# Kernel optimization log

Hardware: AMD Instinct MI355X
Metric: run time of the kernel (lower is better)

## Reference

```python
import jax, jax.numpy as jnp
import numpy as np

B, D, N, K, H = 8, 1024, 4096, 64, 512


def setup_inputs() -> dict:
    key = jax.random.key(0)
    ks = jax.random.split(key, 8)
    s1 = 1.0 / np.sqrt(D)
    s2 = 1.0 / np.sqrt(H)
    return {
        "feature": jax.random.normal(ks[0], (B, D, N), jnp.float32),
        "xyz": jax.random.normal(ks[1], (B, 3, N), jnp.float32),
        "w1": jax.random.normal(ks[2], (H, D), jnp.float32) * s1,
        "b1": jnp.zeros((H,), jnp.float32),
        "g1": jnp.ones((H,), jnp.float32),
        "be1": jnp.zeros((H,), jnp.float32),
        "w2": jax.random.normal(ks[3], (H, H), jnp.float32) * s2,
        "b2": jnp.zeros((H,), jnp.float32),
        "g2": jnp.ones((H,), jnp.float32),
        "be2": jnp.zeros((H,), jnp.float32),
        "w3": jax.random.normal(ks[4], (K, H), jnp.float32) * s2,
        "b3": jnp.zeros((K,), jnp.float32),
    }


def _conv1d(x, w, b):
    # pointwise Conv1d (kernel_size=1): [b,c,n] x [o,c] -> [b,o,n]
    return jnp.einsum('bcn,oc->bon', x, w) + b[None, :, None]


def _bn(x, g, be, eps=1e-5):
    # BatchNorm1d in training mode: batch statistics over (batch, spatial)
    m = x.mean(axis=(0, 2), keepdims=True)
    v = x.var(axis=(0, 2), keepdims=True)
    return (x - m) * jax.lax.rsqrt(v + eps) * g[None, :, None] + be[None, :, None]


def _regular(center, reg=1e-4):
    k = center.shape[-1]
    gram = jnp.einsum('bdm,bdn->bmn', center, center)
    return reg * jnp.abs(gram - jnp.eye(k, dtype=center.dtype)[None]).mean()


def _sinkhorn(cost, epsilon, max_iter):
    # log-domain Sinkhorn with uniform marginals; fixed iteration count
    b, n, m = cost.shape
    log_p = jnp.full((b, n), -np.log(n), cost.dtype)
    log_q = jnp.full((b, m), -np.log(m), cost.dtype)

    def M(u, v):
        return (-cost + u[:, :, None] + v[:, None, :]) / epsilon

    def body(i, uv):
        u, v = uv
        u = epsilon * (log_p - jax.nn.logsumexp(M(u, v), axis=-1)) + u
        v = epsilon * (log_q - jax.nn.logsumexp(M(u, v), axis=-2)) + v
        return (u, v)

    u0 = jnp.zeros((b, n), cost.dtype)
    v0 = jnp.zeros((b, m), cost.dtype)
    u, v = jax.lax.fori_loop(0, max_iter, body, (u0, v0))
    return jnp.exp(M(u, v))  # transport plan gamma [b,n,m]


def _ot_assign(x, y, epsilon=1e-3, max_iter=25, dst='fe'):
    # x: [b,d,n], y: [b,d,m]
    if dst == 'eu':
        xn = jnp.sum(x * x, axis=1)  # [b,n]
        yn = jnp.sum(y * y, axis=1)  # [b,m]
        cost = xn[:, :, None] + yn[:, None, :] - 2.0 * jnp.einsum('bdn,bdm->bnm', x, y)
    else:
        cost = 2.0 - 2.0 * jnp.einsum('bdn,bdm->bnm', x, y)
    return _sinkhorn(cost, epsilon, max_iter)


def _normalize(x, axis=1, eps=1e-12):
    nrm = jnp.linalg.norm(x, axis=axis, keepdims=True)
    return x / jnp.maximum(nrm, eps)


def reference(feature, xyz, w1, b1, g1, be1, w2, b2, g2, be2, w3, b3):
    b, d, n = feature.shape
    h = jax.nn.relu(_bn(_conv1d(feature, w1, b1), g1, be1))
    h = jax.nn.relu(_bn(_conv1d(h, w2, b2), g2, be2))
    log_score = _conv1d(h, w3, b3)  # [b,K,n]
    score = jax.nn.softmax(log_score, axis=1)
    pi = jax.lax.stop_gradient(jnp.maximum(score.sum(-1), 1e-4))[:, None, :]  # [b,1,K]

    # xyz branch
    mu_xyz = jnp.einsum('bkn,bdn->bdk', score, xyz) / pi  # [b,3,K]
    reg_xyz = 0.001 * _regular(mu_xyz)
    gamma_xyz = _ot_assign(jax.lax.stop_gradient(xyz), jax.lax.stop_gradient(mu_xyz), dst='eu')
    assign_xyz = jax.lax.stop_gradient(n * jnp.swapaxes(gamma_xyz, -1, -2))  # [b,K,n]

    # feature branch
    mu_fea = jnp.einsum('bkn,bdn->bdk', score, feature) / pi  # [b,D,K]
    n_feature = _normalize(feature)
    n_mu = _normalize(mu_fea)
    reg_fea = _regular(n_mu)
    gamma_fea = _ot_assign(jax.lax.stop_gradient(n_feature), jax.lax.stop_gradient(n_mu), dst='fe')
    assign_fea = jax.lax.stop_gradient(n * jnp.swapaxes(gamma_fea, -1, -2))  # [b,K,n]

    logp = jax.nn.log_softmax(log_score, axis=1)
    loss_xyz = -jnp.mean(jnp.sum(assign_xyz * logp, axis=1))
    loss_fea = -jnp.mean(jnp.sum(assign_fea * logp, axis=1))
    return loss_xyz + loss_fea + reg_fea + reg_xyz
```

## Files before the change

kernel.cpp:

```cpp
#include <hip/hip_runtime.h>
#include <math.h>

#define B_ 8
#define D_ 1024
#define N_ 4096
#define K_ 64
#define H_ 512

typedef short sx8 __attribute__((ext_vector_type(8)));
typedef float fx4 __attribute__((ext_vector_type(4)));

__device__ __forceinline__ float block_reduce_sum256(float v, float* sm) {
  int tid = threadIdx.x;
  sm[tid] = v;
  __syncthreads();
  for (int s = 128; s > 0; s >>= 1) {
    if (tid < s) sm[tid] += sm[tid + s];
    __syncthreads();
  }
  float r = sm[0];
  __syncthreads();
  return r;
}

__device__ __forceinline__ float bf2f(ushort h) {
  return __uint_as_float(((unsigned)h) << 16);
}
__device__ __forceinline__ void split2(float f, ushort& h, ushort& l) {
  unsigned u = __float_as_uint(f);
  float hf = __uint_as_float(u & 0xffff0000u);
  h = (ushort)(u >> 16);
  l = (ushort)(__float_as_uint(f - hf) >> 16);
}

__global__ __launch_bounds__(256)
void split_w3(const float* __restrict__ W1, const float* __restrict__ W2,
              const float* __restrict__ W3, ushort* __restrict__ Wh1,
              ushort* __restrict__ Wl1, ushort* __restrict__ Wh2,
              ushort* __restrict__ Wl2, ushort* __restrict__ Wh3,
              ushort* __restrict__ Wl3) {
  int i = blockIdx.x * 256 + threadIdx.x;
  const float* W;
  ushort *Wh, *Wl;
  int o;
  if (i < 524288) { W = W1; Wh = Wh1; Wl = Wl1; o = i; }
  else if (i < 786432) { W = W2; Wh = Wh2; Wl = Wl2; o = i - 524288; }
  else { W = W3; Wh = Wh3; Wl = Wl3; o = i - 786432; }
  ushort h, l;
  split2(W[o], h, l);
  Wh[o] = h;
  Wl[o] = l;
}

__global__ __launch_bounds__(256)
void conv_bt128(const ushort* __restrict__ Ah, const ushort* __restrict__ Al,
                const float* __restrict__ Bf, const float* __restrict__ scale,
                const float* __restrict__ shift, float* __restrict__ C,
                const float* __restrict__ bias, float* __restrict__ rs,
                float* __restrict__ rss, float* __restrict__ nrm,
                int Kd, long sB, long sC) {
  __shared__ ushort As[2][128][40];
  __shared__ ushort Bs[2][128][40];
  __shared__ float Ft[32][132];
  __shared__ float scb[32], shb[32];
  __shared__ float rs_l[128], rss_l[128];
  const int t = threadIdx.x;
  const int n0 = blockIdx.x * 128;
  const int m0 = blockIdx.y * 128;
  const int b = blockIdx.z;
  const float* Fsrc = Bf + (long)b * sB;
  float* Cp = C + (long)b * sC;
  const int half = t >> 7, rA = t & 127;
  const ushort* Asrc = (half ? Al : Ah) + (long)(m0 + rA) * Kd;
  ushort* AsD = &As[half][rA][0];
  const int dr = t >> 3, cc = (t & 7) * 16;
  const int nl = t & 127, dh = t >> 7;
  const int w = t >> 6, ln = t & 15, qd = (t & 63) >> 4;
  const int wm = w >> 1, wn = w & 1;
  if (t < 128) { rs_l[t] = 0.f; rss_l[t] = 0.f; }
  float nsq = 0.f;

  fx4 acc[4][4];
#pragma unroll
  for (int i = 0; i < 4; ++i)
#pragma unroll
    for (int j = 0; j < 4; ++j) acc[i][j] = (fx4)0.f;

  for (int k0 = 0; k0 < Kd; k0 += 32) {
    float4 f0 = *(const float4*)(Fsrc + (long)(k0 + dr) * N_ + n0 + cc);
    float4 f1 = *(const float4*)(Fsrc + (long)(k0 + dr) * N_ + n0 + cc + 4);
    float4 f2 = *(const float4*)(Fsrc + (long)(k0 + dr) * N_ + n0 + cc + 8);
    float4 f3 = *(const float4*)(Fsrc + (long)(k0 + dr) * N_ + n0 + cc + 12);
    uint4 a0 = *(const uint4*)(Asrc + k0);
    uint4 a1 = *(const uint4*)(Asrc + k0 + 8);
    uint4 a2 = *(const uint4*)(Asrc + k0 + 16);
    uint4 a3 = *(const uint4*)(Asrc + k0 + 24);
    __syncthreads();
    *(float4*)&Ft[dr][cc] = f0;
    *(float4*)&Ft[dr][cc + 4] = f1;
    *(float4*)&Ft[dr][cc + 8] = f2;
    *(float4*)&Ft[dr][cc + 12] = f3;
    *(uint4*)(AsD + 0) = a0;
    *(uint4*)(AsD + 8) = a1;
    *(uint4*)(AsD + 16) = a2;
    *(uint4*)(AsD + 24) = a3;
    if (t < 32) {
      scb[t] = scale ? scale[k0 + t] : 1.f;
      shb[t] = scale ? shift[k0 + t] : 0.f;
    }
    __syncthreads();
    sx8 hv0, hv1, lv0, lv1;
#pragma unroll
    for (int j = 0; j < 8; ++j) {
      float v = Ft[dh * 16 + j][nl];
      if (scale) v = fmaxf(v * scb[dh * 16 + j] + shb[dh * 16 + j], 0.f);
      nsq += v * v;
      ushort h, l;
      split2(v, h, l);
      hv0[j] = (short)h;
      lv0[j] = (short)l;
    }
#pragma unroll
    for (int j = 0; j < 8; ++j) {
      float v = Ft[dh * 16 + 8 + j][nl];
      if (scale) v = fmaxf(v * scb[dh * 16 + 8 + j] + shb[dh * 16 + 8 + j], 0.f);
      nsq += v * v;
      ushort h, l;
      split2(v, h, l);
      hv1[j] = (short)h;
      lv1[j] = (short)l;
    }
    *(sx8*)&Bs[0][nl][dh * 16] = hv0;
    *(sx8*)&Bs[0][nl][dh * 16 + 8] = hv1;
    *(sx8*)&Bs[1][nl][dh * 16] = lv0;
    *(sx8*)&Bs[1][nl][dh * 16 + 8] = lv1;
    __syncthreads();
    sx8 ahf[4], alf[4], bhf[4], blf[4];
#pragma unroll
    for (int mt = 0; mt < 4; ++mt) {
      ahf[mt] = *(const sx8*)&As[0][wm * 64 + mt * 16 + ln][qd * 8];
      alf[mt] = *(const sx8*)&As[1][wm * 64 + mt * 16 + ln][qd * 8];
    }
#pragma unroll
    for (int nt = 0; nt < 4; ++nt) {
      bhf[nt] = *(const sx8*)&Bs[0][wn * 64 + nt * 16 + ln][qd * 8];
      blf[nt] = *(const sx8*)&Bs[1][wn * 64 + nt * 16 + ln][qd * 8];
    }
#pragma unroll
    for (int mt = 0; mt < 4; ++mt)
#pragma unroll
      for (int nt = 0; nt < 4; ++nt) {
        acc[mt][nt] = __builtin_amdgcn_mfma_f32_16x16x32_bf16(ahf[mt], bhf[nt], acc[mt][nt], 0, 0, 0);
        acc[mt][nt] = __builtin_amdgcn_mfma_f32_16x16x32_bf16(alf[mt], bhf[nt], acc[mt][nt], 0, 0, 0);
        acc[mt][nt] = __builtin_amdgcn_mfma_f32_16x16x32_bf16(ahf[mt], blf[nt], acc[mt][nt], 0, 0, 0);
      }
  }
#pragma unroll
  for (int mt = 0; mt < 4; ++mt) {
#pragma unroll
    for (int rr = 0; rr < 4; ++rr) {
      int rloc = wm * 64 + mt * 16 + qd * 4 + rr;
      int row = m0 + rloc;
      float bb = bias[row];
      float s1 = 0.f, s2 = 0.f;
#pragma unroll
      for (int nt = 0; nt < 4; ++nt) {
        int col = n0 + wn * 64 + nt * 16 + ln;
        float y = acc[mt][nt][rr] + bb;
        Cp[(long)row * N_ + col] = y;
        s1 += y;
        s2 += y * y;
      }
      if (rs) {
#pragma unroll
        for (int m = 1; m < 16; m <<= 1) {
          s1 += __shfl_xor(s1, m);
          s2 += __shfl_xor(s2, m);
        }
        if (ln == 0) {
          atomicAdd(&rs_l[rloc], s1);
          atomicAdd(&rss_l[rloc], s2);
        }
      }
    }
  }
  if (nrm && blockIdx.y == 0)
    atomicAdd(&nrm[(long)b * N_ + n0 + nl], nsq);
  if (rs) {
    __syncthreads();
    if (t < 128) {
      atomicAdd(&rs[m0 + t], rs_l[t]);
      atomicAdd(&rss[m0 + t], rss_l[t]);
    }
  }
}

__global__ void bn_fin(const float* __restrict__ rs, const float* __restrict__ rss,
                       const float* __restrict__ g, const float* __restrict__ be,
                       float* __restrict__ sc, float* __restrict__ sh) {
  int c = blockIdx.x * 256 + threadIdx.x;
  if (c < H_) {
    float inv = 1.f / (float)(B_ * N_);
    float m = rs[c] * inv;
    float var = rss[c] * inv - m * m;
    float s = g[c] * rsqrtf(var + 1e-5f);
    sc[c] = s;
    sh[c] = be[c] - m * s;
  }
}

__global__ __launch_bounds__(256)
void conv64_bn(const ushort* __restrict__ Ah, const ushort* __restrict__ Al,
               const float* __restrict__ Bf, const float* __restrict__ scale,
               const float* __restrict__ shift, float* __restrict__ C,
               const float* __restrict__ bias, int Kd, long sB, long sC) {
  __shared__ ushort As[2][64][40];
  __shared__ ushort Bs[2][128][40];
  __shared__ float Ft[32][132];
  __shared__ float scb[32], shb[32];
  const int t = threadIdx.x;
  const int n0 = blockIdx.x * 128;
  const int b = blockIdx.z;
  const float* Fsrc = Bf + (long)b * sB;
  float* Cp = C + (long)b * sC;
  const bool doA = t < 128;
  const int hA = (t >> 6) & 1, rA = t & 63;
  const ushort* Asrc = (hA ? Al : Ah) + (long)rA * Kd;
  ushort* AsD = &As[hA][rA][0];
  const int dr = t >> 3, cc = (t & 7) * 16;
  const int nl = t & 127, dh = t >> 7;
  const int w = t >> 6, ln = t & 15, qd = (t & 63) >> 4;
  const int wm = w >> 1, wn = w & 1;

  fx4 acc[2][4];
#pragma unroll
  for (int i = 0; i < 2; ++i)
#pragma unroll
    for (int j = 0; j < 4; ++j) acc[i][j] = (fx4)0.f;

  for (int k0 = 0; k0 < Kd; k0 += 32) {
    float4 f0 = *(const float4*)(Fsrc + (long)(k0 + dr) * N_ + n0 + cc);
    float4 f1 = *(const float4*)(Fsrc + (long)(k0 + dr) * N_ + n0 + cc + 4);
    float4 f2 = *(const float4*)(Fsrc + (long)(k0 + dr) * N_ + n0 + cc + 8);
    float4 f3 = *(const float4*)(Fsrc + (long)(k0 + dr) * N_ + n0 + cc + 12);
    uint4 a0, a1, a2, a3;
    if (doA) {
      a0 = *(const uint4*)(Asrc + k0);
      a1 = *(const uint4*)(Asrc + k0 + 8);
      a2 = *(const uint4*)(Asrc + k0 + 16);
      a3 = *(const uint4*)(Asrc + k0 + 24);
    }
    __syncthreads();
    *(float4*)&Ft[dr][cc] = f0;
    *(float4*)&Ft[dr][cc + 4] = f1;
    *(float4*)&Ft[dr][cc + 8] = f2;
    *(float4*)&Ft[dr][cc + 12] = f3;
    if (doA) {
      *(uint4*)(AsD + 0) = a0;
      *(uint4*)(AsD + 8) = a1;
      *(uint4*)(AsD + 16) = a2;
      *(uint4*)(AsD + 24) = a3;
    }
    if (t < 32) {
      scb[t] = scale[k0 + t];
      shb[t] = shift[k0 + t];
    }
    __syncthreads();
    sx8 hv0, hv1, lv0, lv1;
#pragma unroll
    for (int j = 0; j < 8; ++j) {
      float v = Ft[dh * 16 + j][nl];
      v = fmaxf(v * scb[dh * 16 + j] + shb[dh * 16 + j], 0.f);
      ushort h, l;
      split2(v, h, l);
      hv0[j] = (short)h;
      lv0[j] = (short)l;
    }
#pragma unroll
    for (int j = 0; j < 8; ++j) {
      float v = Ft[dh * 16 + 8 + j][nl];
      v = fmaxf(v * scb[dh * 16 + 8 + j] + shb[dh * 16 + 8 + j], 0.f);
      ushort h, l;
      split2(v, h, l);
      hv1[j] = (short)h;
      lv1[j] = (short)l;
    }
    *(sx8*)&Bs[0][nl][dh * 16] = hv0;
    *(sx8*)&Bs[0][nl][dh * 16 + 8] = hv1;
    *(sx8*)&Bs[1][nl][dh * 16] = lv0;
    *(sx8*)&Bs[1][nl][dh * 16 + 8] = lv1;
    __syncthreads();
    sx8 ahf[2], alf[2], bhf[4], blf[4];
#pragma unroll
    for (int mt = 0; mt < 2; ++mt) {
      ahf[mt] = *(const sx8*)&As[0][wm * 32 + mt * 16 + ln][qd * 8];
      alf[mt] = *(const sx8*)&As[1][wm * 32 + mt * 16 + ln][qd * 8];
    }
#pragma unroll
    for (int nt = 0; nt < 4; ++nt) {
      bhf[nt] = *(const sx8*)&Bs[0][wn * 64 + nt * 16 + ln][qd * 8];
      blf[nt] = *(const sx8*)&Bs[1][wn * 64 + nt * 16 + ln][qd * 8];
    }
#pragma unroll
    for (int mt = 0; mt < 2; ++mt)
#pragma unroll
      for (int nt = 0; nt < 4; ++nt) {
        acc[mt][nt] = __builtin_amdgcn_mfma_f32_16x16x32_bf16(ahf[mt], bhf[nt], acc[mt][nt], 0, 0, 0);
        acc[mt][nt] = __builtin_amdgcn_mfma_f32_16x16x32_bf16(alf[mt], bhf[nt], acc[mt][nt], 0, 0, 0);
        acc[mt][nt] = __builtin_amdgcn_mfma_f32_16x16x32_bf16(ahf[mt], blf[nt], acc[mt][nt], 0, 0, 0);
      }
  }
#pragma unroll
  for (int mt = 0; mt < 2; ++mt)
#pragma unroll
    for (int rr = 0; rr < 4; ++rr) {
      int row = wm * 32 + mt * 16 + qd * 4 + rr;
      float bb = bias[row];
#pragma unroll
      for (int nt = 0; nt < 4; ++nt) {
        int col = n0 + wn * 64 + nt * 16 + ln;
        Cp[(long)row * N_ + col] = acc[mt][nt][rr] + bb;
      }
    }
}

__global__ __launch_bounds__(256)
void gemm64_bf(const ushort* __restrict__ Ah, const ushort* __restrict__ Al,
               const float* __restrict__ Bf, float* __restrict__ Cacc) {
  __shared__ ushort As[2][64][40];
  __shared__ ushort Bs[2][128][40];
  const int t = threadIdx.x;
  const int nc0 = blockIdx.x * 128;
  const int kBeg = blockIdx.y * 1024;
  const int b = blockIdx.z;
  const int pc = t >> 7, rB = t & 127;
  const float* Bsrc = Bf + (long)b * D_ * N_ + (long)(nc0 + rB) * N_ + kBeg + pc * 16;
  const bool doA = t < 128;
  const int hA = (t >> 6) & 1, rA = t & 63;
  const ushort* Asrc = (hA ? Al : Ah) + (long)b * K_ * N_ + (long)rA * N_ + kBeg;
  ushort* AsD = &As[hA][rA][0];
  const int w = t >> 6, ln = t & 15, qd = (t & 63) >> 4;
  const int wm = w >> 1, wn = w & 1;

  fx4 acc[2][4];
#pragma unroll
  for (int i = 0; i < 2; ++i)
#pragma unroll
    for (int j = 0; j < 4; ++j) acc[i][j] = (fx4)0.f;

  for (int k0 = 0; k0 < 1024; k0 += 32) {
    float4 f0 = *(const float4*)(Bsrc + k0);
    float4 f1 = *(const float4*)(Bsrc + k0 + 4);
    float4 f2 = *(const float4*)(Bsrc + k0 + 8);
    float4 f3 = *(const float4*)(Bsrc + k0 + 12);
    uint4 a0, a1, a2, a3;
    if (doA) {
      a0 = *(const uint4*)(Asrc + k0);
      a1 = *(const uint4*)(Asrc + k0 + 8);
      a2 = *(const uint4*)(Asrc + k0 + 16);
      a3 = *(const uint4*)(Asrc + k0 + 24);
    }
    float fv[16] = {f0.x, f0.y, f0.z, f0.w, f1.x, f1.y, f1.z, f1.w,
                    f2.x, f2.y, f2.z, f2.w, f3.x, f3.y, f3.z, f3.w};
    sx8 hv0, hv1, lv0, lv1;
#pragma unroll
    for (int j = 0; j < 8; ++j) {
      ushort h, l;
      split2(fv[j], h, l);
      hv0[j] = (short)h;
      lv0[j] = (short)l;
    }
#pragma unroll
    for (int j = 0; j < 8; ++j) {
      ushort h, l;
      split2(fv[8 + j], h, l);
      hv1[j] = (short)h;
      lv1[j] = (short)l;
    }
    __syncthreads();
    *(sx8*)&Bs[0][rB][pc * 16] = hv0;
    *(sx8*)&Bs[0][rB][pc * 16 + 8] = hv1;
    *(sx8*)&Bs[1][rB][pc * 16] = lv0;
    *(sx8*)&Bs[1][rB][pc * 16 + 8] = lv1;
    if (doA) {
      *(uint4*)(AsD + 0) = a0;
      *(uint4*)(AsD + 8) = a1;
      *(uint4*)(AsD + 16) = a2;
      *(uint4*)(AsD + 24) = a3;
    }
    __syncthreads();
    sx8 ahf[2], alf[2], bhf[4], blf[4];
#pragma unroll
    for (int mt = 0; mt < 2; ++mt) {
      ahf[mt] = *(const sx8*)&As[0][wm * 32 + mt * 16 + ln][qd * 8];
      alf[mt] = *(const sx8*)&As[1][wm * 32 + mt * 16 + ln][qd * 8];
    }
#pragma unroll
    for (int nt = 0; nt < 4; ++nt) {
      bhf[nt] = *(const sx8*)&Bs[0][wn * 64 + nt * 16 + ln][qd * 8];
      blf[nt] = *(const sx8*)&Bs[1][wn * 64 + nt * 16 + ln][qd * 8];
    }
#pragma unroll
    for (int mt = 0; mt < 2; ++mt)
#pragma unroll
      for (int nt = 0; nt < 4; ++nt) {
        acc[mt][nt] = __builtin_amdgcn_mfma_f32_16x16x32_bf16(ahf[mt], bhf[nt], acc[mt][nt], 0, 0, 0);
        acc[mt][nt] = __builtin_amdgcn_mfma_f32_16x16x32_bf16(alf[mt], bhf[nt], acc[mt][nt], 0, 0, 0);
        acc[mt][nt] = __builtin_amdgcn_mfma_f32_16x16x32_bf16(ahf[mt], blf[nt], acc[mt][nt], 0, 0, 0);
      }
  }
#pragma unroll
  for (int mt = 0; mt < 2; ++mt)
#pragma unroll
    for (int rr = 0; rr < 4; ++rr) {
      int row = wm * 32 + mt * 16 + qd * 4 + rr;
#pragma unroll
      for (int nt = 0; nt < 4; ++nt) {
        int col = nc0 + wn * 64 + nt * 16 + ln;
        atomicAdd(&Cacc[((long)b * K_ + row) * D_ + col], acc[mt][nt][rr]);
      }
    }
}

__global__ __launch_bounds__(256)
void gemm64_bt(const ushort* __restrict__ Ah, const ushort* __restrict__ Al,
               const float* __restrict__ Bf, const float* __restrict__ nrmsq,
               float* __restrict__ cost) {
  __shared__ ushort As[2][64][40];
  __shared__ ushort Bs[2][128][40];
  __shared__ float Ft[32][132];
  const int t = threadIdx.x;
  const int n0 = blockIdx.x * 128;
  const int b = blockIdx.z;
  const float* Fsrc = Bf + (long)b * D_ * N_;
  const bool doA = t < 128;
  const int hA = (t >> 6) & 1, rA = t & 63;
  const ushort* Asrc = (hA ? Al : Ah) + (long)b * K_ * D_ + (long)rA * D_;
  ushort* AsD = &As[hA][rA][0];
  const int dr = t >> 3, cc = (t & 7) * 16;
  const int nl = t & 127, dh = t >> 7;
  const int w = t >> 6, ln = t & 15, qd = (t & 63) >> 4;
  const int wm = w >> 1, wn = w & 1;

  fx4 acc[2][4];
#pragma unroll
  for (int i = 0; i < 2; ++i)
#pragma unroll
    for (int j = 0; j < 4; ++j) acc[i][j] = (fx4)0.f;

  for (int k0 = 0; k0 < D_; k0 += 32) {
    float4 f0 = *(const float4*)(Fsrc + (long)(k0 + dr) * N_ + n0 + cc);
    float4 f1 = *(const float4*)(Fsrc + (long)(k0 + dr) * N_ + n0 + cc + 4);
    float4 f2 = *(const float4*)(Fsrc + (long)(k0 + dr) * N_ + n0 + cc + 8);
    float4 f3 = *(const float4*)(Fsrc + (long)(k0 + dr) * N_ + n0 + cc + 12);
    uint4 a0, a1, a2, a3;
    if (doA) {
      a0 = *(const uint4*)(Asrc + k0);
      a1 = *(const uint4*)(Asrc + k0 + 8);
      a2 = *(const uint4*)(Asrc + k0 + 16);
      a3 = *(const uint4*)(Asrc + k0 + 24);
    }
    __syncthreads();
    *(float4*)&Ft[dr][cc] = f0;
    *(float4*)&Ft[dr][cc + 4] = f1;
    *(float4*)&Ft[dr][cc + 8] = f2;
    *(float4*)&Ft[dr][cc + 12] = f3;
    if (doA) {
      *(uint4*)(AsD + 0) = a0;
      *(uint4*)(AsD + 8) = a1;
      *(uint4*)(AsD + 16) = a2;
      *(uint4*)(AsD + 24) = a3;
    }
    __syncthreads();
    sx8 hv0, hv1, lv0, lv1;
#pragma unroll
    for (int j = 0; j < 8; ++j) {
      ushort h, l;
      split2(Ft[dh * 16 + j][nl], h, l);
      hv0[j] = (short)h;
      lv0[j] = (short)l;
    }
#pragma unroll
    for (int j = 0; j < 8; ++j) {
      ushort h, l;
      split2(Ft[dh * 16 + 8 + j][nl], h, l);
      hv1[j] = (short)h;
      lv1[j] = (short)l;
    }
    *(sx8*)&Bs[0][nl][dh * 16] = hv0;
    *(sx8*)&Bs[0][nl][dh * 16 + 8] = hv1;
    *(sx8*)&Bs[1][nl][dh * 16] = lv0;
    *(sx8*)&Bs[1][nl][dh * 16 + 8] = lv1;
    __syncthreads();
    sx8 ahf[2], alf[2], bhf[4], blf[4];
#pragma unroll
    for (int mt = 0; mt < 2; ++mt) {
      ahf[mt] = *(const sx8*)&As[0][wm * 32 + mt * 16 + ln][qd * 8];
      alf[mt] = *(const sx8*)&As[1][wm * 32 + mt * 16 + ln][qd * 8];
    }
#pragma unroll
    for (int nt = 0; nt < 4; ++nt) {
      bhf[nt] = *(const sx8*)&Bs[0][wn * 64 + nt * 16 + ln][qd * 8];
      blf[nt] = *(const sx8*)&Bs[1][wn * 64 + nt * 16 + ln][qd * 8];
    }
#pragma unroll
    for (int mt = 0; mt < 2; ++mt)
#pragma unroll
      for (int nt = 0; nt < 4; ++nt) {
        acc[mt][nt] = __builtin_amdgcn_mfma_f32_16x16x32_bf16(ahf[mt], bhf[nt], acc[mt][nt], 0, 0, 0);
        acc[mt][nt] = __builtin_amdgcn_mfma_f32_16x16x32_bf16(alf[mt], bhf[nt], acc[mt][nt], 0, 0, 0);
        acc[mt][nt] = __builtin_amdgcn_mfma_f32_16x16x32_bf16(ahf[mt], blf[nt], acc[mt][nt], 0, 0, 0);
      }
  }
#pragma unroll
  for (int nt = 0; nt < 4; ++nt) {
    int col = n0 + wn * 64 + nt * 16 + ln;
    float q = nrmsq[b * N_ + col];
    float iv = 1.f / fmaxf(sqrtf(q), 1e-12f);
#pragma unroll
    for (int mt = 0; mt < 2; ++mt)
#pragma unroll
      for (int rr = 0; rr < 4; ++rr) {
        int row = wm * 32 + mt * 16 + qd * 4 + rr;
        cost[((long)b * K_ + row) * N_ + col] = 2.f - 2.f * acc[mt][nt][rr] * iv;
      }
  }
}

__global__ __launch_bounds__(256)
void softmax_nk(const float* __restrict__ ls, ushort* __restrict__ sch,
                ushort* __restrict__ scl, float* __restrict__ logpNK,
                float* __restrict__ pi_raw) {
  __shared__ float L[64][65];
  __shared__ float ploc[64];
  int tid = threadIdx.x;
  if (tid < 64) ploc[tid] = 0.f;
  __syncthreads();
  int bi = blockIdx.x >> 4;
  int nb = (blockIdx.x & 15) * 256;
  int n = nb + tid;
  const float* x = ls + ((long)bi * K_) * N_ + n;
  float xv[64];
#pragma unroll
  for (int k = 0; k < 64; ++k) xv[k] = x[(long)k * N_];
  float mx = -1e30f;
#pragma unroll
  for (int k = 0; k < 64; ++k) mx = fmaxf(mx, xv[k]);
  float s = 0.f;
#pragma unroll
  for (int k = 0; k < 64; ++k) s += __expf(xv[k] - mx);
  float lg = __logf(s);
  float inv = 1.f / s;
#pragma unroll
  for (int k = 0; k < 64; ++k) {
    float sc = __expf(xv[k] - mx) * inv;
    long o = ((long)bi * K_ + k) * N_ + n;
    ushort h, l;
    split2(sc, h, l);
    sch[o] = h;
    scl[o] = l;
    atomicAdd(&ploc[k], sc);
  }
  __syncthreads();
  if (tid < 64) atomicAdd(&pi_raw[bi * 64 + tid], ploc[tid]);
  int myw = tid >> 6, nl = tid & 63;
  int row = tid >> 2, ch = (tid & 3) * 16;
  for (int p = 0; p < 4; ++p) {
    __syncthreads();
    if (myw == p) {
#pragma unroll
      for (int k = 0; k < 64; ++k) L[nl][k] = xv[k] - mx - lg;
    }
    __syncthreads();
    float o0[16];
#pragma unroll
    for (int j = 0; j < 16; ++j) o0[j] = L[row][ch + j];
    float* dst = logpNK + ((long)bi * N_ + nb + p * 64 + row) * 64 + ch;
    *(float4*)(dst + 0) = make_float4(o0[0], o0[1], o0[2], o0[3]);
    *(float4*)(dst + 4) = make_float4(o0[4], o0[5], o0[6], o0[7]);
    *(float4*)(dst + 8) = make_float4(o0[8], o0[9], o0[10], o0[11]);
    *(float4*)(dst + 12) = make_float4(o0[12], o0[13], o0[14], o0[15]);
  }
}

__global__ __launch_bounds__(64)
void mu_xyz_k(const ushort* __restrict__ sch, const ushort* __restrict__ scl,
              const float* __restrict__ xyz, const float* __restrict__ pi_raw,
              float* __restrict__ mu, float* __restrict__ yn) {
  int k = blockIdx.x, b = blockIdx.y, t = threadIdx.x;
  const ushort* sh = sch + ((long)b * K_ + k) * N_;
  const ushort* sl = scl + ((long)b * K_ + k) * N_;
  const float* xp = xyz + (long)b * 3 * N_;
  float a0 = 0, a1 = 0, a2 = 0;
  for (int n = t; n < N_; n += 64) {
    float s = bf2f(sh[n]) + bf2f(sl[n]);
    a0 += s * xp[n];
    a1 += s * xp[N_ + n];
    a2 += s * xp[2 * N_ + n];
  }
  for (int off = 32; off > 0; off >>= 1) {
    a0 += __shfl_down(a0, off);
    a1 += __shfl_down(a1, off);
    a2 += __shfl_down(a2, off);
  }
  if (t == 0) {
    float p = fmaxf(pi_raw[b * K_ + k], 1e-4f);
    float m0 = a0 / p, m1 = a1 / p, m2 = a2 / p;
    mu[((long)b * 3 + 0) * K_ + k] = m0;
    mu[((long)b * 3 + 1) * K_ + k] = m1;
    mu[((long)b * 3 + 2) * K_ + k] = m2;
    yn[b * K_ + k] = m0 * m0 + m1 * m1 + m2 * m2;
  }
}

__global__ __launch_bounds__(256)
void reg_xyz_k(const float* __restrict__ mu, float* __restrict__ out) {
  __shared__ float red[256];
  int b = blockIdx.x, tid = threadIdx.x;
  float acc = 0.f;
  for (int e = tid; e < 4096; e += 256) {
    int m = e >> 6, n2 = e & 63;
    float g = 0.f;
    for (int d = 0; d < 3; ++d)
      g += mu[((long)b * 3 + d) * K_ + m] * mu[((long)b * 3 + d) * K_ + n2];
    acc += fabsf(g - (m == n2 ? 1.f : 0.f));
  }
  float tot = block_reduce_sum256(acc, red);
  if (tid == 0) atomicAdd(out, tot * (1e-7f / 32768.f));
}

__global__ __launch_bounds__(256)
void reg_fea_k(const float* __restrict__ nT, float* __restrict__ out) {
  __shared__ float pm[1024];
  __shared__ float red[256];
  int m = blockIdx.x, b = blockIdx.y, tid = threadIdx.x;
  const float* base = nT + (long)b * K_ * D_;
  *(float4*)&pm[tid * 4] = *(const float4*)(base + (long)m * D_ + tid * 4);
  __syncthreads();
  int n2 = tid >> 2, q = tid & 3;
  const float* pn = base + (long)n2 * D_ + q * 256;
  const float* pml = &pm[q * 256];
  float g = 0.f;
#pragma unroll 8
  for (int d = 0; d < 256; d += 4) {
    float4 v = *(const float4*)(pn + d);
    g += v.x * pml[d] + v.y * pml[d + 1] + v.z * pml[d + 2] + v.w * pml[d + 3];
  }
  g += __shfl_down(g, 2);
  g += __shfl_down(g, 1);
  float acc = (q == 0) ? fabsf(g - (m == n2 ? 1.f : 0.f)) : 0.f;
  float tot = block_reduce_sum256(acc, red);
  if (tid == 0) atomicAdd(out, tot * (1e-4f / 32768.f));
}

__global__ __launch_bounds__(256)
void mu_finalize(const float* __restrict__ muT_raw, const float* __restrict__ pi_raw,
                 float* __restrict__ n_muT, ushort* __restrict__ nmu_h,
                 ushort* __restrict__ nmu_l) {
  __shared__ float red[256];
  int k = blockIdx.x, b = blockIdx.y, tid = threadIdx.x;
  float p = fmaxf(pi_raw[b * K_ + k], 1e-4f);
  const float* src = muT_raw + ((long)b * K_ + k) * D_;
  float ss = 0.f;
  for (int d = tid; d < D_; d += 256) {
    float v = src[d] / p;
    ss += v * v;
  }
  float tot = block_reduce_sum256(ss, red);
  float inv = 1.f / fmaxf(sqrtf(tot), 1e-12f);
  long o = ((long)b * K_ + k) * D_;
  for (int d = tid; d < D_; d += 256) {
    float v = src[d] / p * inv;
    n_muT[o + d] = v;
    ushort h, l;
    split2(v, h, l);
    nmu_h[o + d] = h;
    nmu_l[o + d] = l;
  }
}

__global__ __launch_bounds__(256, 1)
void sinkhorn_coop(const float* __restrict__ cost_f, const float* __restrict__ xyz,
                   const float* __restrict__ mu, const float* __restrict__ yn,
                   const float* __restrict__ logpNK, float* __restrict__ out,
                   unsigned long long* __restrict__ partMS,
                   unsigned int* __restrict__ seq) {
  __shared__ float tile[4][64][68];
  __shared__ float vsh[64];
  __shared__ float wm[4][64];
  __shared__ float wsum[4][64];
  __shared__ float red[256];
  __shared__ float mub[4][64];
  const int tid = threadIdx.x;
  const int g = blockIdx.x & 15;
  const int s = blockIdx.x >> 4;
  const int w = tid >> 6, lane = tid & 63;
  const int i = s * 256 + tid;
  const int b = g & 7;
  const float eps = 1e-3f, ti = 1000.0f;
  const float lgp = -8.317766166719343f;
  const float lgq = -4.1588830833596715f;

  float c[64];
  if (g < 8) {
    if (tid < 64) {
      mub[0][tid] = mu[(b * 3 + 0) * K_ + tid];
      mub[1][tid] = mu[(b * 3 + 1) * K_ + tid];
      mub[2][tid] = mu[(b * 3 + 2) * K_ + tid];
      mub[3][tid] = yn[b * K_ + tid];
      vsh[tid] = 0.f;
    }
    __syncthreads();
    float x0 = xyz[((long)b * 3 + 0) * N_ + i];
    float x1 = xyz[((long)b * 3 + 1) * N_ + i];
    float x2 = xyz[((long)b * 3 + 2) * N_ + i];
    float xn = x0 * x0 + x1 * x1 + x2 * x2;
#pragma unroll
    for (int j = 0; j < 64; ++j)
      c[j] = xn + mub[3][j] - 2.f * (x0 * mub[0][j] + x1 * mub[1][j] + x2 * mub[2][j]);
  } else {
    const float* C = cost_f + (long)b * K_ * N_;
#pragma unroll
    for (int j = 0; j < 64; ++j) c[j] = C[(long)j * N_ + i];
    if (tid < 64) vsh[tid] = 0.f;
    __syncthreads();
  }
  float u = 0.f;

  for (int it = 0; it < 25; ++it) {
    float tj[64];
#pragma unroll
    for (int j = 0; j < 64; ++j) tj[j] = vsh[j] - c[j];
    float dm = -1e30f;
#pragma unroll
    for (int j = 0; j < 64; ++j) dm = fmaxf(dm, tj[j]);
    float ssum = 0.f;
#pragma unroll
    for (int j = 0; j < 64; ++j) ssum += __expf((tj[j] - dm) * ti);
    u = eps * (lgp - ((u + dm) * ti + __logf(ssum))) + u;
#pragma unroll
    for (int j4 = 0; j4 < 16; ++j4) {
      float4 v4;
      v4.x = (u + tj[j4 * 4 + 0]) * ti;
      v4.y = (u + tj[j4 * 4 + 1]) * ti;
      v4.z = (u + tj[j4 * 4 + 2]) * ti;
      v4.w = (u + tj[j4 * 4 + 3]) * ti;
      *(float4*)&tile[w][lane][j4 * 4] = v4;
    }
    __syncthreads();
    float M = -1e30f, S = 0.f;
#pragma unroll
    for (int r = 0; r < 64; ++r) {
      float a = tile[w][r][lane];
      M = fmaxf(M, a);
      S += __expf(a - lgp);
    }
    wm[w][lane] = M;
    wsum[w][lane] = S;
    __syncthreads();
    int buf = it & 1;
    if (tid < 64) {
      float Mb = fmaxf(fmaxf(wm[0][tid], wm[1][tid]), fmaxf(wm[2][tid], wm[3][tid]));
      float Sb = wsum[0][tid] + wsum[1][tid] + wsum[2][tid] + wsum[3][tid];
      unsigned long long pk =
          ((unsigned long long)__float_as_uint(Sb) << 32) | (unsigned long long)__float_as_uint(Mb);
      long idx = (((long)buf * 16 + g) * 16 + s) * 64 + tid;
      __hip_atomic_store(&partMS[idx], pk, __ATOMIC_RELAXED, __HIP_MEMORY_SCOPE_AGENT);
    }
    __syncthreads();
    unsigned target = (unsigned)(it + 1);
    if (tid == 0)
      __hip_atomic_store(&seq[((long)g * 16 + s) * 32], target, __ATOMIC_RELEASE,
                         __HIP_MEMORY_SCOPE_AGENT);
    if (tid < 16) {
      while (__hip_atomic_load(&seq[((long)g * 16 + tid) * 32], __ATOMIC_ACQUIRE,
                               __HIP_MEMORY_SCOPE_AGENT) < target)
        __builtin_amdgcn_s_sleep(1);
    }
    __syncthreads();
    if (tid < 64) {
      long base = (((long)buf * 16 + g) * 16) * 64 + tid;
      float M2 = -1e30f, S2 = 0.f;
#pragma unroll
      for (int p = 0; p < 16; ++p) {
        unsigned long long v =
            __hip_atomic_load(&partMS[base + (long)p * 64], __ATOMIC_RELAXED, __HIP_MEMORY_SCOPE_AGENT);
        M2 = fmaxf(M2, __uint_as_float((unsigned)v));
        S2 += __uint_as_float((unsigned)(v >> 32));
      }
      float lsec = fmaxf(M2, lgp + __logf(S2));
      vsh[tid] = eps * (lgq - lsec) + vsh[tid];
    }
    __syncthreads();
  }

  const float* lp = logpNK + ((long)b * N_ + i) * 64;
  float part = 0.f;
#pragma unroll
  for (int j = 0; j < 64; ++j)
    part += __expf((u + vsh[j] - c[j]) * ti) * lp[j];
  red[tid] = part;
  __syncthreads();
  for (int st2 = 128; st2 > 0; st2 >>= 1) {
    if (tid < st2) red[tid] += red[tid + st2];
    __syncthreads();
  }
  if (tid == 0) atomicAdd(out, -red[0] / (float)B_);
}

extern "C" void kernel_launch(void* const* d_in, const int* in_sizes, int n_in,
                              void* d_out, int out_size, void* d_ws, size_t ws_size,
                              hipStream_t stream) {
  const float* feature = (const float*)d_in[0];
  const float* xyz = (const float*)d_in[1];
  const float* w1 = (const float*)d_in[2];
  const float* b1 = (const float*)d_in[3];
  const float* g1 = (const float*)d_in[4];
  const float* be1 = (const float*)d_in[5];
  const float* w2 = (const float*)d_in[6];
  const float* b2 = (const float*)d_in[7];
  const float* g2 = (const float*)d_in[8];
  const float* be2 = (const float*)d_in[9];
  const float* w3 = (const float*)d_in[10];
  const float* b3 = (const float*)d_in[11];
  float* out = (float*)d_out;
  float* ws = (float*)d_ws;

  const long RSZ = 16777216L;
  float* regA = ws;
  float* regB1 = ws + RSZ;
  float* sm = ws + 3 * RSZ;

  float* h1raw = regA;
  float* h2raw = regB1;
  const long sz = (long)B_ * N_ * K_;
  float* log_score = regA;
  float* logpNK = regA + sz;
  float* cost_f = regA + 2 * sz;
  ushort* sc_h = (ushort*)(regA + 3 * sz);
  ushort* sc_l = sc_h + sz;

  ushort* Wh1 = (ushort*)sm; sm += 262144;
  ushort* Wl1 = (ushort*)sm; sm += 262144;
  ushort* Wh2 = (ushort*)sm; sm += 131072;
  ushort* Wl2 = (ushort*)sm; sm += 131072;
  ushort* Wh3 = (ushort*)sm; sm += 16384;
  ushort* Wl3 = (ushort*)sm; sm += 16384;
  float* muT_raw = sm; sm += (long)B_ * K_ * D_;
  float* n_muT = sm;   sm += (long)B_ * K_ * D_;
  ushort* nmu_h = (ushort*)sm; sm += 262144;
  ushort* nmu_l = (ushort*)sm; sm += 262144;
  unsigned long long* partMS = (unsigned long long*)sm; sm += 2 * 16 * 16 * 64 * 2;
  unsigned int* seq = (unsigned int*)sm; sm += 16 * 16 * 32;
  float* nrmsq = sm; sm += (long)B_ * N_;
  float* mu_x = sm;   sm += 2048;
  float* yn = sm;     sm += 512;
  float* pi_raw = sm; sm += 512;
  float* rs1 = sm; sm += 512;
  float* rss1 = sm; sm += 512;
  float* rs2 = sm; sm += 512;
  float* rss2 = sm; sm += 512;
  float* sc1 = sm; sm += 512;
  float* sh1 = sm; sm += 512;
  float* sc2 = sm; sm += 512;
  float* sh2 = sm; sm += 512;

  hipMemsetAsync(d_out, 0, sizeof(float) * out_size, stream);
  hipMemsetAsync(pi_raw, 0, 512 * sizeof(float), stream);
  hipMemsetAsync(seq, 0, 16 * 16 * 32 * sizeof(unsigned int), stream);
  hipMemsetAsync(muT_raw, 0, (long)B_ * K_ * D_ * sizeof(float), stream);
  hipMemsetAsync(nrmsq, 0, (long)B_ * N_ * sizeof(float), stream);
  hipMemsetAsync(rs1, 0, 4 * 512 * sizeof(float), stream);

  split_w3<<<3200, 256, 0, stream>>>(w1, w2, w3, Wh1, Wl1, Wh2, Wl2, Wh3, Wl3);
  {
    dim3 g(N_ / 128, H_ / 128, B_);
    conv_bt128<<<g, 256, 0, stream>>>(Wh1, Wl1, feature, nullptr, nullptr, h1raw,
                                      b1, rs1, rss1, nrmsq, D_, (long)D_ * N_,
                                      (long)H_ * N_);
  }
  bn_fin<<<2, 256, 0, stream>>>(rs1, rss1, g1, be1, sc1, sh1);
  {
    dim3 g(N_ / 128, H_ / 128, B_);
    conv_bt128<<<g, 256, 0, stream>>>(Wh2, Wl2, h1raw, sc1, sh1, h2raw, b2, rs2,
                                      rss2, nullptr, H_, (long)H_ * N_,
                                      (long)H_ * N_);
  }
  bn_fin<<<2, 256, 0, stream>>>(rs2, rss2, g2, be2, sc2, sh2);
  {
    dim3 g(N_ / 128, 1, B_);
    conv64_bn<<<g, 256, 0, stream>>>(Wh3, Wl3, h2raw, sc2, sh2, log_score, b3,
                                     H_, (long)H_ * N_, (long)K_ * N_);
  }
  softmax_nk<<<B_ * N_ / 256, 256, 0, stream>>>(log_score, sc_h, sc_l, logpNK,
                                                pi_raw);
  {
    dim3 g(K_, B_);
    mu_xyz_k<<<g, 64, 0, stream>>>(sc_h, sc_l, xyz, pi_raw, mu_x, yn);
  }
  reg_xyz_k<<<B_, 256, 0, stream>>>(mu_x, out);
  {
    dim3 g(D_ / 128, 4, B_);
    gemm64_bf<<<g, 256, 0, stream>>>(sc_h, sc_l, feature, muT_raw);
  }
  {
    dim3 g(K_, B_);
    mu_finalize<<<g, 256, 0, stream>>>(muT_raw, pi_raw, n_muT, nmu_h, nmu_l);
  }
  {
    dim3 g(K_, B_);
    reg_fea_k<<<g, 256, 0, stream>>>(n_muT, out);
  }
  {
    dim3 g(N_ / 128, 1, B_);
    gemm64_bt<<<g, 256, 0, stream>>>(nmu_h, nmu_l, feature, nrmsq, cost_f);
  }
  {
    void* kargs[] = {(void*)&cost_f, (void*)&xyz, (void*)&mu_x, (void*)&yn,
                     (void*)&logpNK, (void*)&out, (void*)&partMS, (void*)&seq};
    hipLaunchCooperativeKernel((const void*)sinkhorn_coop, dim3(256), dim3(256),
                               kargs, 0, stream);
  }
}
```

Before: 1.050 ms.

## Pre-transpose and split features, run conv chain in point-major layout

Adds a transpose_split kernel that converts the feature tensor once to point-major bf16 hi/lo pairs and computes the squared norms. The three pointwise convolutions are rewritten as conv1n, conv2n and conv3n, which read contiguous rows of point-major activations, so the old per-tile LDS transpose-and-split of the B operand is no longer needed. BN statistics become per-column reductions, and a new softmax_nk2 consumes the transposed logits. This costs an extra pass that writes the split feature copy, and it changes the workspace aliasing, which could introduce buffer conflicts.

New measurement: 1.058 ms. About the same (+0.8%).

```diff
diff --git a/kernel.cpp b/kernel.cpp
--- a/kernel.cpp
+++ b/kernel.cpp
@@ -53,32 +53,69 @@
 }
 
 __global__ __launch_bounds__(256)
-void conv_bt128(const ushort* __restrict__ Ah, const ushort* __restrict__ Al,
-                const float* __restrict__ Bf, const float* __restrict__ scale,
-                const float* __restrict__ shift, float* __restrict__ C,
-                const float* __restrict__ bias, float* __restrict__ rs,
-                float* __restrict__ rss, float* __restrict__ nrm,
-                int Kd, long sB, long sC) {
+void transpose_split(const float* __restrict__ F, ushort* __restrict__ FhT,
+                     ushort* __restrict__ FlT, float* __restrict__ nrmsq) {
+  __shared__ float tile[64][65];
+  __shared__ float nsq[64];
+  int b = blockIdx.z, d0 = blockIdx.y * 64, n0 = blockIdx.x * 64;
+  const float* src = F + ((long)b * D_ + d0) * N_ + n0;
+  int t = threadIdx.x;
+  if (t < 64) nsq[t] = 0.f;
+  int rr4 = t >> 4, c4 = (t & 15) * 4;
+#pragma unroll
+  for (int p = 0; p < 4; ++p) {
+    int dr = p * 16 + rr4;
+    float4 v = *(const float4*)(src + (long)dr * N_ + c4);
+    tile[dr][c4 + 0] = v.x;
+    tile[dr][c4 + 1] = v.y;
+    tile[dr][c4 + 2] = v.z;
+    tile[dr][c4 + 3] = v.w;
+  }
+  __syncthreads();
+  int nlb = t >> 3, ds = (t & 7) * 8;
+#pragma unroll
+  for (int p = 0; p < 2; ++p) {
+    int nl = p * 32 + nlb;
+    sx8 hv, lv;
+    float sq = 0.f;
+#pragma unroll
+    for (int j = 0; j < 8; ++j) {
+      float f = tile[ds + j][nl];
+      sq += f * f;
+      ushort h, l;
+      split2(f, h, l);
+      hv[j] = (short)h;
+      lv[j] = (short)l;
+    }
+    atomicAdd(&nsq[nl], sq);
+    long o = ((long)b * N_ + n0 + nl) * D_ + d0 + ds;
+    *(sx8*)(FhT + o) = hv;
+    *(sx8*)(FlT + o) = lv;
+  }
+  __syncthreads();
+  if (t < 64) atomicAdd(&nrmsq[(long)b * N_ + n0 + t], nsq[t]);
+}
+
+__global__ __launch_bounds__(256)
+void conv1n(const ushort* __restrict__ Ah, const ushort* __restrict__ Al,
+            const ushort* __restrict__ Bh, const ushort* __restrict__ Bl,
+            float* __restrict__ C, const float* __restrict__ bias,
+            float* __restrict__ rs, float* __restrict__ rss) {
   __shared__ ushort As[2][128][40];
   __shared__ ushort Bs[2][128][40];
-  __shared__ float Ft[32][132];
-  __shared__ float scb[32], shb[32];
-  __shared__ float rs_l[128], rss_l[128];
+  __shared__ float st1[128], st2[128];
   const int t = threadIdx.x;
-  const int n0 = blockIdx.x * 128;
-  const int m0 = blockIdx.y * 128;
+  const int c0 = blockIdx.x * 128;
+  const int p0 = blockIdx.y * 128;
   const int b = blockIdx.z;
-  const float* Fsrc = Bf + (long)b * sB;
-  float* Cp = C + (long)b * sC;
-  const int half = t >> 7, rA = t & 127;
-  const ushort* Asrc = (half ? Al : Ah) + (long)(m0 + rA) * Kd;
-  ushort* AsD = &As[half][rA][0];
-  const int dr = t >> 3, cc = (t & 7) * 16;
-  const int nl = t & 127, dh = t >> 7;
+  const int half = t >> 7, r = t & 127;
+  const ushort* Asrc = (half ? Al : Ah) + ((long)b * N_ + p0 + r) * D_;
+  const ushort* Bsrc = (half ? Bl : Bh) + (long)(c0 + r) * D_;
+  ushort* AsD = &As[half][r][0];
+  ushort* BsD = &Bs[half][r][0];
   const int w = t >> 6, ln = t & 15, qd = (t & 63) >> 4;
   const int wm = w >> 1, wn = w & 1;
-  if (t < 128) { rs_l[t] = 0.f; rss_l[t] = 0.f; }
-  float nsq = 0.f;
+  if (t < 128) { st1[t] = 0.f; st2[t] = 0.f; }
 
   fx4 acc[4][4];
 #pragma unroll
@@ -86,54 +123,24 @@
 #pragma unroll
     for (int j = 0; j < 4; ++j) acc[i][j] = (fx4)0.f;
 
-  for (int k0 = 0; k0 < Kd; k0 += 32) {
-    float4 f0 = *(const float4*)(Fsrc + (long)(k0 + dr) * N_ + n0 + cc);
-    float4 f1 = *(const float4*)(Fsrc + (long)(k0 + dr) * N_ + n0 + cc + 4);
-    float4 f2 = *(const float4*)(Fsrc + (long)(k0 + dr) * N_ + n0 + cc + 8);
-    float4 f3 = *(const float4*)(Fsrc + (long)(k0 + dr) * N_ + n0 + cc + 12);
+  for (int k0 = 0; k0 < D_; k0 += 32) {
     uint4 a0 = *(const uint4*)(Asrc + k0);
     uint4 a1 = *(const uint4*)(Asrc + k0 + 8);
     uint4 a2 = *(const uint4*)(Asrc + k0 + 16);
     uint4 a3 = *(const uint4*)(Asrc + k0 + 24);
-    __syncthreads();
-    *(float4*)&Ft[dr][cc] = f0;
-    *(float4*)&Ft[dr][cc + 4] = f1;
-    *(float4*)&Ft[dr][cc + 8] = f2;
-    *(float4*)&Ft[dr][cc + 12] = f3;
+    uint4 b0 = *(const uint4*)(Bsrc + k0);
+    uint4 b1 = *(const uint4*)(Bsrc + k0 + 8);
+    uint4 b2 = *(const uint4*)(Bsrc + k0 + 16);
+    uint4 b3 = *(const uint4*)(Bsrc + k0 + 24);
+    __syncthreads();
     *(uint4*)(AsD + 0) = a0;
     *(uint4*)(AsD + 8) = a1;
     *(uint4*)(AsD + 16) = a2;
     *(uint4*)(AsD + 24) = a3;
-    if (t < 32) {
-      scb[t] = scale ? scale[k0 + t] : 1.f;
-      shb[t] = scale ? shift[k0 + t] : 0.f;
-    }
-    __syncthreads();
-    sx8 hv0, hv1, lv0, lv1;
-#pragma unroll
-    for (int j = 0; j < 8; ++j) {
-      float v = Ft[dh * 16 + j][nl];
-      if (scale) v = fmaxf(v * scb[dh * 16 + j] + shb[dh * 16 + j], 0.f);
-      nsq += v * v;
-      ushort h, l;
-      split2(v, h, l);
-      hv0[j] = (short)h;
-      lv0[j] = (short)l;
-    }
-#pragma unroll
-    for (int j = 0; j < 8; ++j) {
-      float v = Ft[dh * 16 + 8 + j][nl];
-      if (scale) v = fmaxf(v * scb[dh * 16 + 8 + j] + shb[dh * 16 + 8 + j], 0.f);
-      nsq += v * v;
-      ushort h, l;
-      split2(v, h, l);
-      hv1[j] = (short)h;
-      lv1[j] = (short)l;
-    }
-    *(sx8*)&Bs[0][nl][dh * 16] = hv0;
-    *(sx8*)&Bs[0][nl][dh * 16 + 8] = hv1;
-    *(sx8*)&Bs[1][nl][dh * 16] = lv0;
-    *(sx8*)&Bs[1][nl][dh * 16 + 8] = lv1;
+    *(uint4*)(BsD + 0) = b0;
+    *(uint4*)(BsD + 8) = b1;
+    *(uint4*)(BsD + 16) = b2;
+    *(uint4*)(BsD + 24) = b3;
     __syncthreads();
     sx8 ahf[4], alf[4], bhf[4], blf[4];
 #pragma unroll
@@ -155,43 +162,39 @@
         acc[mt][nt] = __builtin_amdgcn_mfma_f32_16x16x32_bf16(ahf[mt], blf[nt], acc[mt][nt], 0, 0, 0);
       }
   }
-#pragma unroll
-  for (int mt = 0; mt < 4; ++mt) {
+  float* Cp = C + (long)b * N_ * H_;
+  float bb[4];
+#pragma unroll
+  for (int nt = 0; nt < 4; ++nt) bb[nt] = bias[c0 + wn * 64 + nt * 16 + ln];
+  float s1[4] = {0, 0, 0, 0}, s2[4] = {0, 0, 0, 0};
+#pragma unroll
+  for (int mt = 0; mt < 4; ++mt)
 #pragma unroll
     for (int rr = 0; rr < 4; ++rr) {
-      int rloc = wm * 64 + mt * 16 + qd * 4 + rr;
-      int row = m0 + rloc;
-      float bb = bias[row];
-      float s1 = 0.f, s2 = 0.f;
+      int p = p0 + wm * 64 + mt * 16 + qd * 4 + rr;
 #pragma unroll
       for (int nt = 0; nt < 4; ++nt) {
-        int col = n0 + wn * 64 + nt * 16 + ln;
-        float y = acc[mt][nt][rr] + bb;
-        Cp[(long)row * N_ + col] = y;
-        s1 += y;
-        s2 += y * y;
+        int ch = c0 + wn * 64 + nt * 16 + ln;
+        float y = acc[mt][nt][rr] + bb[nt];
+        Cp[(long)p * H_ + ch] = y;
+        s1[nt] += y;
+        s2[nt] += y * y;
       }
-      if (rs) {
-#pragma unroll
-        for (int m = 1; m < 16; m <<= 1) {
-          s1 += __shfl_xor(s1, m);
-          s2 += __shfl_xor(s2, m);
-        }
-        if (ln == 0) {
-          atomicAdd(&rs_l[rloc], s1);
-          atomicAdd(&rss_l[rloc], s2);
-        }
-      }
-    }
-  }
-  if (nrm && blockIdx.y == 0)
-    atomicAdd(&nrm[(long)b * N_ + n0 + nl], nsq);
-  if (rs) {
-    __syncthreads();
-    if (t < 128) {
-      atomicAdd(&rs[m0 + t], rs_l[t]);
-      atomicAdd(&rss[m0 + t], rss_l[t]);
-    }
+    }
+#pragma unroll
+  for (int nt = 0; nt < 4; ++nt) {
+    float a = s1[nt], q = s2[nt];
+    a += __shfl_xor(a, 16); a += __shfl_xor(a, 32);
+    q += __shfl_xor(q, 16); q += __shfl_xor(q, 32);
+    if (qd == 0) {
+      atomicAdd(&st1[wn * 64 + nt * 16 + ln], a);
+      atomicAdd(&st2[wn * 64 + nt * 16 + ln], q);
+    }
+  }
+  __syncthreads();
+  if (t < 128) {
+    atomicAdd(&rs[c0 + t], st1[t]);
+    atomicAdd(&rss[c0 + t], st2[t]);
   }
 }
 
@@ -210,67 +213,51 @@
 }
 
 __global__ __launch_bounds__(256)
-void conv64_bn(const ushort* __restrict__ Ah, const ushort* __restrict__ Al,
-               const float* __restrict__ Bf, const float* __restrict__ scale,
-               const float* __restrict__ shift, float* __restrict__ C,
-               const float* __restrict__ bias, int Kd, long sB, long sC) {
-  __shared__ ushort As[2][64][40];
+void conv2n(const float* __restrict__ Aprev, const ushort* __restrict__ Bh,
+            const ushort* __restrict__ Bl, const float* __restrict__ scale,
+            const float* __restrict__ shift, float* __restrict__ C,
+            const float* __restrict__ bias, float* __restrict__ rs,
+            float* __restrict__ rss, int Kd) {
+  __shared__ ushort As[2][128][40];
   __shared__ ushort Bs[2][128][40];
-  __shared__ float Ft[32][132];
-  __shared__ float scb[32], shb[32];
+  __shared__ float scb[512], shb[512];
+  __shared__ float st1[128], st2[128];
   const int t = threadIdx.x;
-  const int n0 = blockIdx.x * 128;
+  const int c0 = blockIdx.x * 128;
+  const int p0 = blockIdx.y * 128;
   const int b = blockIdx.z;
-  const float* Fsrc = Bf + (long)b * sB;
-  float* Cp = C + (long)b * sC;
-  const bool doA = t < 128;
-  const int hA = (t >> 6) & 1, rA = t & 63;
-  const ushort* Asrc = (hA ? Al : Ah) + (long)rA * Kd;
-  ushort* AsD = &As[hA][rA][0];
-  const int dr = t >> 3, cc = (t & 7) * 16;
-  const int nl = t & 127, dh = t >> 7;
+  const int rA = t >> 1, ko = (t & 1) * 16;
+  const float* Asrc = Aprev + ((long)b * N_ + p0 + rA) * Kd + ko;
+  const int halfB = t >> 7, rB = t & 127;
+  const ushort* Bsrc = (halfB ? Bl : Bh) + (long)(c0 + rB) * Kd;
+  ushort* BsD = &Bs[halfB][rB][0];
   const int w = t >> 6, ln = t & 15, qd = (t & 63) >> 4;
   const int wm = w >> 1, wn = w & 1;
-
-  fx4 acc[2][4];
-#pragma unroll
-  for (int i = 0; i < 2; ++i)
+  for (int i = t; i < Kd; i += 256) { scb[i] = scale[i]; shb[i] = shift[i]; }
+  if (t < 128) { st1[t] = 0.f; st2[t] = 0.f; }
+  __syncthreads();
+
+  fx4 acc[4][4];
+#pragma unroll
+  for (int i = 0; i < 4; ++i)
 #pragma unroll
     for (int j = 0; j < 4; ++j) acc[i][j] = (fx4)0.f;
 
   for (int k0 = 0; k0 < Kd; k0 += 32) {
-    float4 f0 = *(const float4*)(Fsrc + (long)(k0 + dr) * N_ + n0 + cc);
-    float4 f1 = *(const float4*)(Fsrc + (long)(k0 + dr) * N_ + n0 + cc + 4);
-    float4 f2 = *(const float4*)(Fsrc + (long)(k0 + dr) * N_ + n0 + cc + 8);
-    float4 f3 = *(const float4*)(Fsrc + (long)(k0 + dr) * N_ + n0 + cc + 12);
-    uint4 a0, a1, a2, a3;
-    if (doA) {
-      a0 = *(const uint4*)(Asrc + k0);
-      a1 = *(const uint4*)(Asrc + k0 + 8);
-      a2 = *(const uint4*)(Asrc + k0 + 16);
-      a3 = *(const uint4*)(Asrc + k0 + 24);
-    }
-    __syncthreads();
-    *(float4*)&Ft[dr][cc] = f0;
-    *(float4*)&Ft[dr][cc + 4] = f1;
-    *(float4*)&Ft[dr][cc + 8] = f2;
-    *(float4*)&Ft[dr][cc + 12] = f3;
-    if (doA) {
-      *(uint4*)(AsD + 0) = a0;
-      *(uint4*)(AsD + 8) = a1;
-      *(uint4*)(AsD + 16) = a2;
-      *(uint4*)(AsD + 24) = a3;
-    }
-    if (t < 32) {
-      scb[t] = scale[k0 + t];
-      shb[t] = shift[k0 + t];
-    }
-    __syncthreads();
+    float4 f0 = *(const float4*)(Asrc + k0);
+    float4 f1 = *(const float4*)(Asrc + k0 + 4);
+    float4 f2 = *(const float4*)(Asrc + k0 + 8);
+    float4 f3 = *(const float4*)(Asrc + k0 + 12);
+    uint4 b0 = *(const uint4*)(Bsrc + k0);
+    uint4 b1 = *(const uint4*)(Bsrc + k0 + 8);
+    uint4 b2 = *(const uint4*)(Bsrc + k0 + 16);
+    uint4 b3 = *(const uint4*)(Bsrc + k0 + 24);
+    float fv[16] = {f0.x, f0.y, f0.z, f0.w, f1.x, f1.y, f1.z, f1.w,
+                    f2.x, f2.y, f2.z, f2.w, f3.x, f3.y, f3.z, f3.w};
     sx8 hv0, hv1, lv0, lv1;
 #pragma unroll
     for (int j = 0; j < 8; ++j) {
-      float v = Ft[dh * 16 + j][nl];
-      v = fmaxf(v * scb[dh * 16 + j] + shb[dh * 16 + j], 0.f);
+      float v = fmaxf(fv[j] * scb[k0 + ko + j] + shb[k0 + ko + j], 0.f);
       ushort h, l;
       split2(v, h, l);
       hv0[j] = (short)h;
@@ -278,23 +265,27 @@
     }
 #pragma unroll
     for (int j = 0; j < 8; ++j) {
-      float v = Ft[dh * 16 + 8 + j][nl];
-      v = fmaxf(v * scb[dh * 16 + 8 + j] + shb[dh * 16 + 8 + j], 0.f);
+      float v = fmaxf(fv[8 + j] * scb[k0 + ko + 8 + j] + shb[k0 + ko + 8 + j], 0.f);
       ushort h, l;
       split2(v, h, l);
       hv1[j] = (short)h;
       lv1[j] = (short)l;
     }
-    *(sx8*)&Bs[0][nl][dh * 16] = hv0;
-    *(sx8*)&Bs[0][nl][dh * 16 + 8] = hv1;
-    *(sx8*)&Bs[1][nl][dh * 16] = lv0;
-    *(sx8*)&Bs[1][nl][dh * 16 + 8] = lv1;
-    __syncthreads();
-    sx8 ahf[2], alf[2], bhf[4], blf[4];
-#pragma unroll
-    for (int mt = 0; mt < 2; ++mt) {
-      ahf[mt] = *(const sx8*)&As[0][wm * 32 + mt * 16 + ln][qd * 8];
-      alf[mt] = *(const sx8*)&As[1][wm * 32 + mt * 16 + ln][qd * 8];
+    __syncthreads();
+    *(sx8*)&As[0][rA][ko] = hv0;
+    *(sx8*)&As[0][rA][ko + 8] = hv1;
+    *(sx8*)&As[1][rA][ko] = lv0;
+    *(sx8*)&As[1][rA][ko + 8] = lv1;
+    *(uint4*)(BsD + 0) = b0;
+    *(uint4*)(BsD + 8) = b1;
+    *(uint4*)(BsD + 16) = b2;
+    *(uint4*)(BsD + 24) = b3;
+    __syncthreads();
+    sx8 ahf[4], alf[4], bhf[4], blf[4];
+#pragma unroll
+    for (int mt = 0; mt < 4; ++mt) {
+      ahf[mt] = *(const sx8*)&As[0][wm * 64 + mt * 16 + ln][qd * 8];
+      alf[mt] = *(const sx8*)&As[1][wm * 64 + mt * 16 + ln][qd * 8];
     }
 #pragma unroll
     for (int nt = 0; nt < 4; ++nt) {
@@ -302,7 +293,7 @@
       blf[nt] = *(const sx8*)&Bs[1][wn * 64 + nt * 16 + ln][qd * 8];
     }
 #pragma unroll
-    for (int mt = 0; mt < 2; ++mt)
+    for (int mt = 0; mt < 4; ++mt)
 #pragma unroll
       for (int nt = 0; nt < 4; ++nt) {
         acc[mt][nt] = __builtin_amdgcn_mfma_f32_16x16x32_bf16(ahf[mt], bhf[nt], acc[mt][nt], 0, 0, 0);
@@ -310,18 +301,267 @@
         acc[mt][nt] = __builtin_amdgcn_mfma_f32_16x16x32_bf16(ahf[mt], blf[nt], acc[mt][nt], 0, 0, 0);
       }
   }
+  float* Cp = C + (long)b * N_ * H_;
+  float bb[4];
+#pragma unroll
+  for (int nt = 0; nt < 4; ++nt) bb[nt] = bias[c0 + wn * 64 + nt * 16 + ln];
+  float s1[4] = {0, 0, 0, 0}, s2[4] = {0, 0, 0, 0};
+#pragma unroll
+  for (int mt = 0; mt < 4; ++mt)
+#pragma unroll
+    for (int rr = 0; rr < 4; ++rr) {
+      int p = p0 + wm * 64 + mt * 16 + qd * 4 + rr;
+#pragma unroll
+      for (int nt = 0; nt < 4; ++nt) {
+        int ch = c0 + wn * 64 + nt * 16 + ln;
+        float y = acc[mt][nt][rr] + bb[nt];
+        Cp[(long)p * H_ + ch] = y;
+        s1[nt] += y;
+        s2[nt] += y * y;
+      }
+    }
+#pragma unroll
+  for (int nt = 0; nt < 4; ++nt) {
+    float a = s1[nt], q = s2[nt];
+    a += __shfl_xor(a, 16); a += __shfl_xor(a, 32);
+    q += __shfl_xor(q, 16); q += __shfl_xor(q, 32);
+    if (qd == 0) {
+      atomicAdd(&st1[wn * 64 + nt * 16 + ln], a);
+      atomicAdd(&st2[wn * 64 + nt * 16 + ln], q);
+    }
+  }
+  __syncthreads();
+  if (t < 128) {
+    atomicAdd(&rs[c0 + t], st1[t]);
+    atomicAdd(&rss[c0 + t], st2[t]);
+  }
+}
+
+__global__ __launch_bounds__(256)
+void conv3n(const float* __restrict__ Aprev, const ushort* __restrict__ Bh,
+            const ushort* __restrict__ Bl, const float* __restrict__ scale,
+            const float* __restrict__ shift, float* __restrict__ C,
+            const float* __restrict__ bias, int Kd) {
+  __shared__ ushort As[2][128][40];
+  __shared__ ushort Bs[2][64][40];
+  __shared__ float scb[512], shb[512];
+  const int t = threadIdx.x;
+  const int p0 = blockIdx.y * 128;
+  const int b = blockIdx.z;
+  const int rA = t >> 1, ko = (t & 1) * 16;
+  const float* Asrc = Aprev + ((long)b * N_ + p0 + rA) * Kd + ko;
+  const bool doB = t < 128;
+  const int halfB = (t >> 6) & 1, rB = t & 63;
+  const ushort* Bsrc = (halfB ? Bl : Bh) + (long)rB * Kd;
+  ushort* BsD = &Bs[halfB][rB][0];
+  const int w = t >> 6, ln = t & 15, qd = (t & 63) >> 4;
+  for (int i = t; i < Kd; i += 256) { scb[i] = scale[i]; shb[i] = shift[i]; }
+  __syncthreads();
+
+  fx4 acc[2][4];
+#pragma unroll
+  for (int i = 0; i < 2; ++i)
+#pragma unroll
+    for (int j = 0; j < 4; ++j) acc[i][j] = (fx4)0.f;
+
+  for (int k0 = 0; k0 < Kd; k0 += 32) {
+    float4 f0 = *(const float4*)(Asrc + k0);
+    float4 f1 = *(const float4*)(Asrc + k0 + 4);
+    float4 f2 = *(const float4*)(Asrc + k0 + 8);
+    float4 f3 = *(const float4*)(Asrc + k0 + 12);
+    uint4 b0, b1, b2, b3;
+    if (doB) {
+      b0 = *(const uint4*)(Bsrc + k0);
+      b1 = *(const uint4*)(Bsrc + k0 + 8);
+      b2 = *(const uint4*)(Bsrc + k0 + 16);
+      b3 = *(const uint4*)(Bsrc + k0 + 24);
+    }
+    float fv[16] = {f0.x, f0.y, f0.z, f0.w, f1.x, f1.y, f1.z, f1.w,
+                    f2.x, f2.y, f2.z, f2.w, f3.x, f3.y, f3.z, f3.w};
+    sx8 hv0, hv1, lv0, lv1;
+#pragma unroll
+    for (int j = 0; j < 8; ++j) {
+      float v = fmaxf(fv[j] * scb[k0 + ko + j] + shb[k0 + ko + j], 0.f);
+      ushort h, l;
+      split2(v, h, l);
+      hv0[j] = (short)h;
+      lv0[j] = (short)l;
+    }
+#pragma unroll
+    for (int j = 0; j < 8; ++j) {
+      float v = fmaxf(fv[8 + j] * scb[k0 + ko + 8 + j] + shb[k0 + ko + 8 + j], 0.f);
+      ushort h, l;
+      split2(v, h, l);
+      hv1[j] = (short)h;
+      lv1[j] = (short)l;
+    }
+    __syncthreads();
+    *(sx8*)&As[0][rA][ko] = hv0;
+    *(sx8*)&As[0][rA][ko + 8] = hv1;
+    *(sx8*)&As[1][rA][ko] = lv0;
+    *(sx8*)&As[1][rA][ko + 8] = lv1;
+    if (doB) {
+      *(uint4*)(BsD + 0) = b0;
+      *(uint4*)(BsD + 8) = b1;
+      *(uint4*)(BsD + 16) = b2;
+      *(uint4*)(BsD + 24) = b3;
+    }
+    __syncthreads();
+    sx8 ahf[2], alf[2], bhf[4], blf[4];
+#pragma unroll
+    for (int mt = 0; mt < 2; ++mt) {
+      ahf[mt] = *(const sx8*)&As[0][w * 32 + mt * 16 + ln][qd * 8];
+      alf[mt] = *(const sx8*)&As[1][w * 32 + mt * 16 + ln][qd * 8];
+    }
+#pragma unroll
+    for (int nt = 0; nt < 4; ++nt) {
+      bhf[nt] = *(const sx8*)&Bs[0][nt * 16 + ln][qd * 8];
+      blf[nt] = *(const sx8*)&Bs[1][nt * 16 + ln][qd * 8];
+    }
+#pragma unroll
+    for (int mt = 0; mt < 2; ++mt)
+#pragma unroll
+      for (int nt = 0; nt < 4; ++nt) {
+        acc[mt][nt] = __builtin_amdgcn_mfma_f32_16x16x32_bf16(ahf[mt], bhf[nt], acc[mt][nt], 0, 0, 0);
+        acc[mt][nt] = __builtin_amdgcn_mfma_f32_16x16x32_bf16(alf[mt], bhf[nt], acc[mt][nt], 0, 0, 0);
+        acc[mt][nt] = __builtin_amdgcn_mfma_f32_16x16x32_bf16(ahf[mt], blf[nt], acc[mt][nt], 0, 0, 0);
+      }
+  }
+  float* Cp = C + (long)b * N_ * 64;
 #pragma unroll
   for (int mt = 0; mt < 2; ++mt)
 #pragma unroll
     for (int rr = 0; rr < 4; ++rr) {
-      int row = wm * 32 + mt * 16 + qd * 4 + rr;
-      float bb = bias[row];
+      int p = p0 + w * 32 + mt * 16 + qd * 4 + rr;
 #pragma unroll
       for (int nt = 0; nt < 4; ++nt) {
-        int col = n0 + wn * 64 + nt * 16 + ln;
-        Cp[(long)row * N_ + col] = acc[mt][nt][rr] + bb;
+        int ch = nt * 16 + ln;
+        Cp[(long)p * 64 + ch] = acc[mt][nt][rr] + bias[ch];
       }
     }
+}
+
+__global__ __launch_bounds__(256)
+void softmax_nk2(const float* __restrict__ lsT, ushort* __restrict__ sch,
+                 ushort* __restrict__ scl, float* __restrict__ logpNK,
+                 float* __restrict__ pi_raw) {
+  __shared__ float ploc[64];
+  int tid = threadIdx.x;
+  if (tid < 64) ploc[tid] = 0.f;
+  __syncthreads();
+  int bi = blockIdx.x >> 4;
+  int n = (blockIdx.x & 15) * 256 + tid;
+  long gp = (long)bi * N_ + n;
+  const float* x = lsT + gp * 64;
+  float xv[64];
+#pragma unroll
+  for (int j4 = 0; j4 < 16; ++j4) {
+    float4 v = *(const float4*)(x + j4 * 4);
+    xv[j4 * 4 + 0] = v.x;
+    xv[j4 * 4 + 1] = v.y;
+    xv[j4 * 4 + 2] = v.z;
+    xv[j4 * 4 + 3] = v.w;
+  }
+  float mx = -1e30f;
+#pragma unroll
+  for (int k = 0; k < 64; ++k) mx = fmaxf(mx, xv[k]);
+  float s = 0.f;
+#pragma unroll
+  for (int k = 0; k < 64; ++k) s += __expf(xv[k] - mx);
+  float lg = __logf(s);
+  float inv = 1.f / s;
+#pragma unroll
+  for (int k = 0; k < 64; ++k) {
+    float sc = __expf(xv[k] - mx) * inv;
+    long o = ((long)bi * K_ + k) * N_ + n;
+    ushort h, l;
+    split2(sc, h, l);
+    sch[o] = h;
+    scl[o] = l;
+    atomicAdd(&ploc[k], sc);
+  }
+  float* lp = logpNK + gp * 64;
+#pragma unroll
+  for (int j4 = 0; j4 < 16; ++j4) {
+    float4 o;
+    o.x = xv[j4 * 4 + 0] - mx - lg;
+    o.y = xv[j4 * 4 + 1] - mx - lg;
+    o.z = xv[j4 * 4 + 2] - mx - lg;
+    o.w = xv[j4 * 4 + 3] - mx - lg;
+    *(float4*)(lp + j4 * 4) = o;
+  }
+  __syncthreads();
+  if (tid < 64) atomicAdd(&pi_raw[bi * 64 + tid], ploc[tid]);
+}
+
+__global__ __launch_bounds__(64)
+void mu_xyz_k(const ushort* __restrict__ sch, const ushort* __restrict__ scl,
+              const float* __restrict__ xyz, const float* __restrict__ pi_raw,
+              float* __restrict__ mu, float* __restrict__ yn) {
+  int k = blockIdx.x, b = blockIdx.y, t = threadIdx.x;
+  const ushort* sh = sch + ((long)b * K_ + k) * N_;
+  const ushort* sl = scl + ((long)b * K_ + k) * N_;
+  const float* xp = xyz + (long)b * 3 * N_;
+  float a0 = 0, a1 = 0, a2 = 0;
+  for (int n = t; n < N_; n += 64) {
+    float s = bf2f(sh[n]) + bf2f(sl[n]);
+    a0 += s * xp[n];
+    a1 += s * xp[N_ + n];
+    a2 += s * xp[2 * N_ + n];
+  }
+  for (int off = 32; off > 0; off >>= 1) {
+    a0 += __shfl_down(a0, off);
+    a1 += __shfl_down(a1, off);
+    a2 += __shfl_down(a2, off);
+  }
+  if (t == 0) {
+    float p = fmaxf(pi_raw[b * K_ + k], 1e-4f);
+    float m0 = a0 / p, m1 = a1 / p, m2 = a2 / p;
+    mu[((long)b * 3 + 0) * K_ + k] = m0;
+    mu[((long)b * 3 + 1) * K_ + k] = m1;
+    mu[((long)b * 3 + 2) * K_ + k] = m2;
+    yn[b * K_ + k] = m0 * m0 + m1 * m1 + m2 * m2;
+  }
+}
+
+__global__ __launch_bounds__(256)
+void reg_xyz_k(const float* __restrict__ mu, float* __restrict__ out) {
+  __shared__ float red[256];
+  int b = blockIdx.x, tid = threadIdx.x;
+  float acc = 0.f;
+  for (int e = tid; e < 4096; e += 256) {
+    int m = e >> 6, n2 = e & 63;
+    float g = 0.f;
+    for (int d = 0; d < 3; ++d)
+      g += mu[((long)b * 3 + d) * K_ + m] * mu[((long)b * 3 + d) * K_ + n2];
+    acc += fabsf(g - (m == n2 ? 1.f : 0.f));
+  }
+  float tot = block_reduce_sum256(acc, red);
+  if (tid == 0) atomicAdd(out, tot * (1e-7f / 32768.f));
+}
+
+__global__ __launch_bounds__(256)
+void reg_fea_k(const float* __restrict__ nT, float* __restrict__ out) {
+  __shared__ float pm[1024];
+  __shared__ float red[256];
+  int m = blockIdx.x, b = blockIdx.y, tid = threadIdx.x;
+  const float* base = nT + (long)b * K_ * D_;
+  *(float4*)&pm[tid * 4] = *(const float4*)(base + (long)m * D_ + tid * 4);
+  __syncthreads();
+  int n2 = tid >> 2, q = tid & 3;
+  const float* pn = base + (long)n2 * D_ + q * 256;
+  const float* pml = &pm[q * 256];
+  float g = 0.f;
+#pragma unroll 8
+  for (int d = 0; d < 256; d += 4) {
+    float4 v = *(const float4*)(pn + d);
+    g += v.x * pml[d] + v.y * pml[d + 1] + v.z * pml[d + 2] + v.w * pml[d + 3];
+  }
+  g += __shfl_down(g, 2);
+  g += __shfl_down(g, 1);
+  float acc = (q == 0) ? fabsf(g - (m == n2 ? 1.f : 0.f)) : 0.f;
+  float tot = block_reduce_sum256(acc, red);
+  if (tid == 0) atomicAdd(out, tot * (1e-4f / 32768.f));
 }
 
 __global__ __launch_bounds__(256)
@@ -420,6 +660,32 @@
         atomicAdd(&Cacc[((long)b * K_ + row) * D_ + col], acc[mt][nt][rr]);
       }
     }
+}
+
+__global__ __launch_bounds__(256)
+void mu_finalize(const float* __restrict__ muT_raw, const float* __restrict__ pi_raw,
+                 float* __restrict__ n_muT, ushort* __restrict__ nmu_h,
+                 ushort* __restrict__ nmu_l) {
+  __shared__ float red[256];
+  int k = blockIdx.x, b = blockIdx.y, tid = threadIdx.x;
+  float p = fmaxf(pi_raw[b * K_ + k], 1e-4f);
+  const float* src = muT_raw + ((long)b * K_ + k) * D_;
+  float ss = 0.f;
+  for (int d = tid; d < D_; d += 256) {
+    float v = src[d] / p;
+    ss += v * v;
+  }
+  float tot = block_reduce_sum256(ss, red);
+  float inv = 1.f / fmaxf(sqrtf(tot), 1e-12f);
+  long o = ((long)b * K_ + k) * D_;
+  for (int d = tid; d < D_; d += 256) {
+    float v = src[d] / p * inv;
+    n_muT[o + d] = v;
+    ushort h, l;
+    split2(v, h, l);
+    nmu_h[o + d] = h;
+    nmu_l[o + d] = l;
+  }
 }
 
 __global__ __launch_bounds__(256)
@@ -524,158 +790,6 @@
         int row = wm * 32 + mt * 16 + qd * 4 + rr;
         cost[((long)b * K_ + row) * N_ + col] = 2.f - 2.f * acc[mt][nt][rr] * iv;
       }
-  }
-}
-
-__global__ __launch_bounds__(256)
-void softmax_nk(const float* __restrict__ ls, ushort* __restrict__ sch,
-                ushort* __restrict__ scl, float* __restrict__ logpNK,
-                float* __restrict__ pi_raw) {
-  __shared__ float L[64][65];
-  __shared__ float ploc[64];
-  int tid = threadIdx.x;
-  if (tid < 64) ploc[tid] = 0.f;
-  __syncthreads();
-  int bi = blockIdx.x >> 4;
-  int nb = (blockIdx.x & 15) * 256;
-  int n = nb + tid;
-  const float* x = ls + ((long)bi * K_) * N_ + n;
-  float xv[64];
-#pragma unroll
-  for (int k = 0; k < 64; ++k) xv[k] = x[(long)k * N_];
-  float mx = -1e30f;
-#pragma unroll
-  for (int k = 0; k < 64; ++k) mx = fmaxf(mx, xv[k]);
-  float s = 0.f;
-#pragma unroll
-  for (int k = 0; k < 64; ++k) s += __expf(xv[k] - mx);
-  float lg = __logf(s);
-  float inv = 1.f / s;
-#pragma unroll
-  for (int k = 0; k < 64; ++k) {
-    float sc = __expf(xv[k] - mx) * inv;
-    long o = ((long)bi * K_ + k) * N_ + n;
-    ushort h, l;
-    split2(sc, h, l);
-    sch[o] = h;
-    scl[o] = l;
-    atomicAdd(&ploc[k], sc);
-  }
-  __syncthreads();
-  if (tid < 64) atomicAdd(&pi_raw[bi * 64 + tid], ploc[tid]);
-  int myw = tid >> 6, nl = tid & 63;
-  int row = tid >> 2, ch = (tid & 3) * 16;
-  for (int p = 0; p < 4; ++p) {
-    __syncthreads();
-    if (myw == p) {
-#pragma unroll
-      for (int k = 0; k < 64; ++k) L[nl][k] = xv[k] - mx - lg;
-    }
-    __syncthreads();
-    float o0[16];
-#pragma unroll
-    for (int j = 0; j < 16; ++j) o0[j] = L[row][ch + j];
-    float* dst = logpNK + ((long)bi * N_ + nb + p * 64 + row) * 64 + ch;
-    *(float4*)(dst + 0) = make_float4(o0[0], o0[1], o0[2], o0[3]);
-    *(float4*)(dst + 4) = make_float4(o0[4], o0[5], o0[6], o0[7]);
-    *(float4*)(dst + 8) = make_float4(o0[8], o0[9], o0[10], o0[11]);
-    *(float4*)(dst + 12) = make_float4(o0[12], o0[13], o0[14], o0[15]);
-  }
-}
-
-__global__ __launch_bounds__(64)
-void mu_xyz_k(const ushort* __restrict__ sch, const ushort* __restrict__ scl,
-              const float* __restrict__ xyz, const float* __restrict__ pi_raw,
-              float* __restrict__ mu, float* __restrict__ yn) {
-  int k = blockIdx.x, b = blockIdx.y, t = threadIdx.x;
-  const ushort* sh = sch + ((long)b * K_ + k) * N_;
-  const ushort* sl = scl + ((long)b * K_ + k) * N_;
-  const float* xp = xyz + (long)b * 3 * N_;
-  float a0 = 0, a1 = 0, a2 = 0;
-  for (int n = t; n < N_; n += 64) {
-    float s = bf2f(sh[n]) + bf2f(sl[n]);
-    a0 += s * xp[n];
-    a1 += s * xp[N_ + n];
-    a2 += s * xp[2 * N_ + n];
-  }
-  for (int off = 32; off > 0; off >>= 1) {
-    a0 += __shfl_down(a0, off);
-    a1 += __shfl_down(a1, off);
-    a2 += __shfl_down(a2, off);
-  }
-  if (t == 0) {
-    float p = fmaxf(pi_raw[b * K_ + k], 1e-4f);
-    float m0 = a0 / p, m1 = a1 / p, m2 = a2 / p;
-    mu[((long)b * 3 + 0) * K_ + k] = m0;
-    mu[((long)b * 3 + 1) * K_ + k] = m1;
-    mu[((long)b * 3 + 2) * K_ + k] = m2;
-    yn[b * K_ + k] = m0 * m0 + m1 * m1 + m2 * m2;
-  }
-}
-
-__global__ __launch_bounds__(256)
-void reg_xyz_k(const float* __restrict__ mu, float* __restrict__ out) {
-  __shared__ float red[256];
-  int b = blockIdx.x, tid = threadIdx.x;
-  float acc = 0.f;
-  for (int e = tid; e < 4096; e += 256) {
-    int m = e >> 6, n2 = e & 63;
-    float g = 0.f;
-    for (int d = 0; d < 3; ++d)
-      g += mu[((long)b * 3 + d) * K_ + m] * mu[((long)b * 3 + d) * K_ + n2];
-    acc += fabsf(g - (m == n2 ? 1.f : 0.f));
-  }
-  float tot = block_reduce_sum256(acc, red);
-  if (tid == 0) atomicAdd(out, tot * (1e-7f / 32768.f));
-}
-
-__global__ __launch_bounds__(256)
-void reg_fea_k(const float* __restrict__ nT, float* __restrict__ out) {
-  __shared__ float pm[1024];
-  __shared__ float red[256];
-  int m = blockIdx.x, b = blockIdx.y, tid = threadIdx.x;
-  const float* base = nT + (long)b * K_ * D_;
-  *(float4*)&pm[tid * 4] = *(const float4*)(base + (long)m * D_ + tid * 4);
-  __syncthreads();
-  int n2 = tid >> 2, q = tid & 3;
-  const float* pn = base + (long)n2 * D_ + q * 256;
-  const float* pml = &pm[q * 256];
-  float g = 0.f;
-#pragma unroll 8
-  for (int d = 0; d < 256; d += 4) {
-    float4 v = *(const float4*)(pn + d);
-    g += v.x * pml[d] + v.y * pml[d + 1] + v.z * pml[d + 2] + v.w * pml[d + 3];
-  }
-  g += __shfl_down(g, 2);
-  g += __shfl_down(g, 1);
-  float acc = (q == 0) ? fabsf(g - (m == n2 ? 1.f : 0.f)) : 0.f;
-  float tot = block_reduce_sum256(acc, red);
-  if (tid == 0) atomicAdd(out, tot * (1e-4f / 32768.f));
-}
-
-__global__ __launch_bounds__(256)
-void mu_finalize(const float* __restrict__ muT_raw, const float* __restrict__ pi_raw,
-                 float* __restrict__ n_muT, ushort* __restrict__ nmu_h,
-                 ushort* __restrict__ nmu_l) {
-  __shared__ float red[256];
-  int k = blockIdx.x, b = blockIdx.y, tid = threadIdx.x;
-  float p = fmaxf(pi_raw[b * K_ + k], 1e-4f);
-  const float* src = muT_raw + ((long)b * K_ + k) * D_;
-  float ss = 0.f;
-  for (int d = tid; d < D_; d += 256) {
-    float v = src[d] / p;
-    ss += v * v;
-  }
-  float tot = block_reduce_sum256(ss, red);
-  float inv = 1.f / fmaxf(sqrtf(tot), 1e-12f);
-  long o = ((long)b * K_ + k) * D_;
-  for (int d = tid; d < D_; d += 256) {
-    float v = src[d] / p * inv;
-    n_muT[o + d] = v;
-    ushort h, l;
-    split2(v, h, l);
-    nmu_h[o + d] = h;
-    nmu_l[o + d] = l;
   }
 }
 
@@ -827,18 +941,21 @@
   float* ws = (float*)d_ws;
 
   const long RSZ = 16777216L;
-  float* regA = ws;
-  float* regB1 = ws + RSZ;
+  float* reg0 = ws;
+  float* reg1 = ws + RSZ;
+  float* reg2 = ws + 2 * RSZ;
   float* sm = ws + 3 * RSZ;
 
-  float* h1raw = regA;
-  float* h2raw = regB1;
+  ushort* FhT = (ushort*)reg0;
+  ushort* FlT = (ushort*)reg1;
+  float* h1T = reg2;
+  float* h2T = reg0;
   const long sz = (long)B_ * N_ * K_;
-  float* log_score = regA;
-  float* logpNK = regA + sz;
-  float* cost_f = regA + 2 * sz;
-  ushort* sc_h = (ushort*)(regA + 3 * sz);
+  float* log_scoreT = reg1;
+  float* logpNK = reg1 + sz;
+  ushort* sc_h = (ushort*)(reg1 + 2 * sz);
   ushort* sc_l = sc_h + sz;
+  float* cost_f = reg1 + 4 * sz;
 
   ushort* Wh1 = (ushort*)sm; sm += 262144;
   ushort* Wl1 = (ushort*)sm; sm += 262144;
@@ -874,26 +991,25 @@
 
   split_w3<<<3200, 256, 0, stream>>>(w1, w2, w3, Wh1, Wl1, Wh2, Wl2, Wh3, Wl3);
   {
-    dim3 g(N_ / 128, H_ / 128, B_);
-    conv_bt128<<<g, 256, 0, stream>>>(Wh1, Wl1, feature, nullptr, nullptr, h1raw,
-                                      b1, rs1, rss1, nrmsq, D_, (long)D_ * N_,
-                                      (long)H_ * N_);
+    dim3 g(N_ / 64, D_ / 64, B_);
+    transpose_split<<<g, 256, 0, stream>>>(feature, FhT, FlT, nrmsq);
+  }
+  {
+    dim3 g(H_ / 128, N_ / 128, B_);
+    conv1n<<<g, 256, 0, stream>>>(FhT, FlT, Wh1, Wl1, h1T, b1, rs1, rss1);
   }
   bn_fin<<<2, 256, 0, stream>>>(rs1, rss1, g1, be1, sc1, sh1);
   {
-    dim3 g(N_ / 128, H_ / 128, B_);
-    conv_bt128<<<g, 256, 0, stream>>>(Wh2, Wl2, h1raw, sc1, sh1, h2raw, b2, rs2,
-                                      rss2, nullptr, H_, (long)H_ * N_,
-                                      (long)H_ * N_);
+    dim3 g(H_ / 128, N_ / 128, B_);
+    conv2n<<<g, 256, 0, stream>>>(h1T, Wh2, Wl2, sc1, sh1, h2T, b2, rs2, rss2, H_);
   }
   bn_fin<<<2, 256, 0, stream>>>(rs2, rss2, g2, be2, sc2, sh2);
   {
-    dim3 g(N_ / 128, 1, B_);
-    conv64_bn<<<g, 256, 0, stream>>>(Wh3, Wl3, h2raw, sc2, sh2, log_score, b3,
-                                     H_, (long)H_ * N_, (long)K_ * N_);
-  }
-  softmax_nk<<<B_ * N_ / 256, 256, 0, stream>>>(log_score, sc_h, sc_l, logpNK,
-                                                pi_raw);
+    dim3 g(1, N_ / 128, B_);
+    conv3n<<<g, 256, 0, stream>>>(h2T, Wh3, Wl3, sc2, sh2, log_scoreT, b3, H_);
+  }
+  softmax_nk2<<<B_ * N_ / 256, 256, 0, stream>>>(log_scoreT, sc_h, sc_l, logpNK,
+                                                 pi_raw);
   {
     dim3 g(K_, B_);
     mu_xyz_k<<<g, 64, 0, stream>>>(sc_h, sc_l, xyz, pi_raw, mu_x, yn);
```
